# Kernel optimization log

Measured on AMD Instinct MI355X. Metric: run time of the kernel, lower is better.

## Reference

```python
import jax, jax.numpy as jnp
import numpy as np

IN_DIM = 512
OUT_DIM = 512
NUM_HARMONICS = 32
BATCH = 4096


def setup_inputs() -> dict:
    key = jax.random.key(0)
    k1, k2 = jax.random.split(key)
    x = jax.random.normal(k1, (BATCH, IN_DIM), dtype=jnp.float32)
    std = 1.0 / np.sqrt(IN_DIM * NUM_HARMONICS)
    fourier_coeffs = jax.random.normal(
        k2, (IN_DIM, NUM_HARMONICS, 2, OUT_DIM), dtype=jnp.float32) * std
    bias = jnp.zeros((OUT_DIM,), dtype=jnp.float32)
    return {"x": x, "fourier_coeffs": fourier_coeffs, "bias": bias}


def reference(x, fourier_coeffs, bias):
    # k = [1, ..., num_harmonics]
    k = jnp.arange(1, fourier_coeffs.shape[1] + 1, dtype=x.dtype)
    kx = x[:, :, None] * k                      # [b, i, g]
    trig = jnp.stack([jnp.cos(kx), jnp.sin(kx)], axis=-1)  # [b, i, g, 2]
    out = jnp.einsum('bigf,igfo->bo', trig, fourier_coeffs)
    return out + bias
```

## Files before the change

kernel.cpp:

```cpp
#include <hip/hip_runtime.h>
#include <hip/hip_bf16.h>
#include <stdint.h>
#include <stddef.h>

#define BATCH   4096
#define INDIM   512
#define OUTDIM  512
#define NH      32
#define KKDIM   64
#define INV2PI  0.15915494309189535f

#define BM       256
#define BN       256
#define THREADS  512
#define KSPLIT   8
#define DIMS_PER_WG (INDIM / KSPLIT)
#define CHUNK_ELEMS (BN * KKDIM)

#define B_BYTES   32768
#define A_BYTES   (BM * 128)
#define OFF_A0    (2 * B_BYTES)
#define OFF_X     (OFF_A0 + 2 * A_BYTES)
#define X_CHUNK_BYTES (8 * BM * 4)
#define SMEM_BYTES (OFF_X + 2 * X_CHUNK_BYTES)

typedef short  bhalf8  __attribute__((ext_vector_type(8)));
typedef float  vfloat4 __attribute__((ext_vector_type(4)));

__device__ __forceinline__ unsigned pack_bf16(float a, float b) {
    union { __hip_bfloat162 h2; unsigned u; } cv;
    cv.h2 = __float22bfloat162_rn(float2{a, b});
    return cv.u;
}

__device__ __forceinline__ void async_copy16(const void* gsrc, void* ldst) {
    __builtin_amdgcn_global_load_lds(
        (const __attribute__((address_space(1))) void*)(uintptr_t)gsrc,
        (__attribute__((address_space(3))) void*)(uint32_t)(uintptr_t)ldst,
        16, 0, 0);
}

__global__ __launch_bounds__(256) void fkan_prepass(const float* __restrict__ coeffs,
                                                    unsigned short* __restrict__ Bt) {
    __shared__ float lds[64][260];
    const int t  = threadIdx.x;
    const int cb = blockIdx.x & 1;
    const int i  = blockIdx.x >> 1;
    const float* __restrict__ src = coeffs + (size_t)i * (KKDIM * OUTDIM) + cb * BN;
    unsigned short* __restrict__ chunk = Bt + (size_t)(cb * INDIM + i) * CHUNK_ELEMS;
#pragma unroll
    for (int rd = 0; rd < 16; ++rd) {
        const int r  = rd * 4 + (t >> 6);
        const int c4 = (t & 63) * 4;
        const float4 v = *(const float4*)(src + (size_t)r * OUTDIM + c4);
        *(float4*)&lds[r][c4] = v;
    }
    __syncthreads();
#pragma unroll
    for (int s = 0; s < 8; ++s) {
        const int unit = t + s * 256;
        const int col  = unit >> 3;
        const int pc   = unit & 7;
        const int kb   = (pc ^ (col & 7)) * 8;
        uint4 o;
        o.x = pack_bf16(lds[kb + 0][col], lds[kb + 1][col]);
        o.y = pack_bf16(lds[kb + 2][col], lds[kb + 3][col]);
        o.z = pack_bf16(lds[kb + 4][col], lds[kb + 5][col]);
        o.w = pack_bf16(lds[kb + 6][col], lds[kb + 7][col]);
        ((uint4*)chunk)[unit] = o;
    }
}

__global__ __launch_bounds__(256) void fkan_bias_init(const float* __restrict__ bias,
                                                      float* __restrict__ out) {
    const int idx = blockIdx.x * 256 + threadIdx.x;
    ((float4*)out)[idx] = ((const float4*)bias)[idx & 127];
}

__device__ __forceinline__ void stage_B(const unsigned short* __restrict__ Bt, char* smem,
                                        int cb, int dim_global, int parity, int t) {
    const char* chunk = (const char*)(Bt + (size_t)(cb * INDIM + dim_global) * CHUNK_ELEMS);
    char* bdst = smem + parity * B_BYTES;
#pragma unroll
    for (int s = 0; s < 4; ++s) {
        const int unit = t + s * 512;
        async_copy16(chunk + unit * 16, bdst + unit * 16);
    }
}

__device__ __forceinline__ void stage_x(const float* __restrict__ x, char* smem,
                                        int rowbase, int dimbase, int cn, int t) {
    const int r  = t >> 1;
    const int d0 = (t & 1) * 4;
    const float4 xv = *(const float4*)(x + (size_t)(rowbase + r) * INDIM + dimbase + cn * 8 + d0);
    float* xr = (float*)(smem + OFF_X + (cn & 1) * X_CHUNK_BYTES);
    xr[(d0 + 0) * BM + r] = xv.x * INV2PI;
    xr[(d0 + 1) * BM + r] = xv.y * INV2PI;
    xr[(d0 + 2) * BM + r] = xv.z * INV2PI;
    xr[(d0 + 3) * BM + r] = xv.w * INV2PI;
}

__device__ __forceinline__ void do_trig(char* smem, int dim_local, int parity, int trow, int tq) {
    const float rv = ((const float*)(smem + OFF_X + ((dim_local >> 3) & 1) * X_CHUNK_BYTES))
                     [(dim_local & 7) * BM + trow];
    const float cd = __builtin_amdgcn_cosf(rv);
    const float sd = __builtin_amdgcn_sinf(rv);
    const float a0 = (float)(tq * 16 + 1) * rv;
    float c = __builtin_amdgcn_cosf(a0);
    float s = __builtin_amdgcn_sinf(a0);
    unsigned pk[16];
    pk[0] = pack_bf16(c, s);
#pragma unroll
    for (int j = 1; j < 16; ++j) {
        const float nc = c * cd - s * sd;
        const float ns = s * cd + c * sd;
        c = nc; s = ns;
        pk[j] = pack_bf16(c, s);
    }
    uint4* abase = (uint4*)(smem + OFF_A0 + parity * A_BYTES + trow * 128);
    const int sw = trow & 7;
    uint4 w0; w0.x = pk[0];  w0.y = pk[1];  w0.z = pk[2];  w0.w = pk[3];
    uint4 w1; w1.x = pk[4];  w1.y = pk[5];  w1.z = pk[6];  w1.w = pk[7];
    uint4 w2; w2.x = pk[8];  w2.y = pk[9];  w2.z = pk[10]; w2.w = pk[11];
    uint4 w3; w3.x = pk[12]; w3.y = pk[13]; w3.z = pk[14]; w3.w = pk[15];
    abase[(tq * 4 + 0) ^ sw] = w0;
    abase[(tq * 4 + 1) ^ sw] = w1;
    abase[(tq * 4 + 2) ^ sw] = w2;
    abase[(tq * 4 + 3) ^ sw] = w3;
}

__global__ __launch_bounds__(THREADS, 2) void fkan_main(const float* __restrict__ x,
                                                        const unsigned short* __restrict__ Bt,
                                                        float* __restrict__ out) {
    __shared__ char smem[SMEM_BYTES];
    const int t      = threadIdx.x;
    const int grp    = blockIdx.x & 15;
    const int member = blockIdx.x >> 4;
    const int cb      = grp & 1;
    const int kq      = grp >> 1;
    const int rowbase = member * BM;
    const int colbase = cb * BN;
    const int dimbase = kq * DIMS_PER_WG;

    const int lane = t & 63;
    const int w    = t >> 6;
    const int wr   = w >> 2;
    const int wc   = w & 3;
    const int fr   = lane & 15;
    const int fq   = lane >> 4;
    const int fx   = lane & 7;

    const int trow = t >> 1;
    const int tq   = t & 1;

    vfloat4 acc[8][4];
#pragma unroll
    for (int a = 0; a < 8; ++a)
#pragma unroll
        for (int b = 0; b < 4; ++b) acc[a][b] = (vfloat4)0.0f;

    stage_x(x, smem, rowbase, dimbase, 0, t);
    __syncthreads();
    stage_B(Bt, smem, cb, dimbase + 0, 0, t);
    do_trig(smem, 0, 0, trow, tq);
    __syncthreads();

#pragma unroll 2
    for (int it = 0; it < DIMS_PER_WG; ++it) {
        const int p    = it & 1;
        const int inxt = it + 1;
        if (inxt < DIMS_PER_WG) {
            stage_B(Bt, smem, cb, dimbase + inxt, inxt & 1, t);
            if ((it & 7) == 0) {
                const int cn = (it >> 3) + 1;
                if (cn < 8) stage_x(x, smem, rowbase, dimbase, cn, t);
            }
            do_trig(smem, inxt, inxt & 1, trow, tq);
        }
        {
            const char* Ab = smem + OFF_A0 + p * A_BYTES;
            const char* Bb = smem + p * B_BYTES;
#pragma unroll
            for (int ks = 0; ks < 2; ++ks) {
                bhalf8 bv[4];
#pragma unroll
                for (int ct = 0; ct < 4; ++ct)
                    bv[ct] = *(const bhalf8*)(Bb + (wc * 64 + ct * 16 + fr) * 128
                                                 + (((ks * 4 + fq) ^ fx) * 16));
#pragma unroll
                for (int rt = 0; rt < 8; ++rt) {
                    const bhalf8 av = *(const bhalf8*)(Ab + (wr * 128 + rt * 16 + fr) * 128
                                                          + (((ks * 4 + fq) ^ fx) * 16));
#pragma unroll
                    for (int ct = 0; ct < 4; ++ct)
                        acc[rt][ct] = __builtin_amdgcn_mfma_f32_16x16x32_bf16(
                            av, bv[ct], acc[rt][ct], 0, 0, 0);
                }
            }
        }
        __syncthreads();
    }

#pragma unroll
    for (int rt = 0; rt < 8; ++rt) {
#pragma unroll
        for (int ct = 0; ct < 4; ++ct) {
            const int col  = colbase + wc * 64 + ct * 16 + fr;
            const int row0 = rowbase + wr * 128 + rt * 16 + fq * 4;
#pragma unroll
            for (int r = 0; r < 4; ++r)
                atomicAdd(out + (size_t)(row0 + r) * OUTDIM + col, acc[rt][ct][r]);
        }
    }
}

__global__ __launch_bounds__(256) void fkan_naive(const float* __restrict__ x,
                                                  const float* __restrict__ coeffs,
                                                  const float* __restrict__ bias,
                                                  float* __restrict__ out) {
    const int b = blockIdx.x >> 1;
    const int o = ((blockIdx.x & 1) << 8) + threadIdx.x;
    float acc = bias[o];
    const float* xrow = x + (size_t)b * INDIM;
    for (int i = 0; i < INDIM; ++i) {
        const float rv = xrow[i] * INV2PI;
        const float cd = __builtin_amdgcn_cosf(rv);
        const float sd = __builtin_amdgcn_sinf(rv);
        float c = cd, s = sd;
        const float* cp = coeffs + (size_t)i * (KKDIM * OUTDIM) + o;
#pragma unroll 4
        for (int g = 0; g < NH; ++g) {
            acc += c * cp[g * 2 * OUTDIM] + s * cp[(g * 2 + 1) * OUTDIM];
            const float nc = c * cd - s * sd;
            const float ns = s * cd + c * sd;
            c = nc; s = ns;
        }
    }
    out[(size_t)b * OUTDIM + o] = acc;
}

extern "C" void kernel_launch(void* const* d_in, const int* in_sizes, int n_in,
                              void* d_out, int out_size, void* d_ws, size_t ws_size,
                              hipStream_t stream) {
    (void)in_sizes; (void)n_in; (void)out_size;
    const float* x      = (const float*)d_in[0];
    const float* coeffs = (const float*)d_in[1];
    const float* bias   = (const float*)d_in[2];
    float* out          = (float*)d_out;

    const size_t bt_bytes = (size_t)2 * INDIM * CHUNK_ELEMS * sizeof(unsigned short);
    if (ws_size >= bt_bytes) {
        unsigned short* Bt = (unsigned short*)d_ws;
        fkan_prepass<<<2 * INDIM, 256, 0, stream>>>(coeffs, Bt);
        fkan_bias_init<<<(BATCH * OUTDIM) / (4 * 256), 256, 0, stream>>>(bias, out);
        fkan_main<<<(BATCH / BM) * 2 * KSPLIT, THREADS, 0, stream>>>(x, Bt, out);
    } else {
        fkan_naive<<<BATCH * 2, 256, 0, stream>>>(x, coeffs, bias, out);
    }
}
```

Baseline: 277.1 us.

## Shrink tiles to 128x128 and load B fragments directly from global memory

Tiles shrink from 256x256 with 512 threads to 128x128 with 256 threads, and the grid grows to 1024 workgroups with a target of four per CU. B is no longer staged in LDS through async copies. Each wave loads its bf16 MFMA fragments straight from global memory, so the prepass drops its XOR swizzle. The change also adds s_setprio around the MFMA block, trading data reuse per tile for more occupancy and less LDS traffic and risking extra global and L2 load pressure.

```diff
diff --git a/kernel.cpp b/kernel.cpp
--- a/kernel.cpp
+++ b/kernel.cpp
@@ -10,19 +10,18 @@
 #define KKDIM   64
 #define INV2PI  0.15915494309189535f
 
-#define BM       256
-#define BN       256
-#define THREADS  512
+#define BM       128
+#define BN       128
+#define THREADS  256
 #define KSPLIT   8
 #define DIMS_PER_WG (INDIM / KSPLIT)
-#define CHUNK_ELEMS (BN * KKDIM)
-
-#define B_BYTES   32768
-#define A_BYTES   (BM * 128)
-#define OFF_A0    (2 * B_BYTES)
-#define OFF_X     (OFF_A0 + 2 * A_BYTES)
+#define CHUNK_COLS  256
+#define CHUNK_ELEMS (CHUNK_COLS * KKDIM)
+
+#define A_BYTES       (BM * 128)
+#define OFF_X         (2 * A_BYTES)
 #define X_CHUNK_BYTES (8 * BM * 4)
-#define SMEM_BYTES (OFF_X + 2 * X_CHUNK_BYTES)
+#define SMEM_BYTES    (OFF_X + 2 * X_CHUNK_BYTES)
 
 typedef short  bhalf8  __attribute__((ext_vector_type(8)));
 typedef float  vfloat4 __attribute__((ext_vector_type(4)));
@@ -31,13 +30,6 @@
     union { __hip_bfloat162 h2; unsigned u; } cv;
     cv.h2 = __float22bfloat162_rn(float2{a, b});
     return cv.u;
-}
-
-__device__ __forceinline__ void async_copy16(const void* gsrc, void* ldst) {
-    __builtin_amdgcn_global_load_lds(
-        (const __attribute__((address_space(1))) void*)(uintptr_t)gsrc,
-        (__attribute__((address_space(3))) void*)(uint32_t)(uintptr_t)ldst,
-        16, 0, 0);
 }
 
 __global__ __launch_bounds__(256) void fkan_prepass(const float* __restrict__ coeffs,
@@ -46,7 +38,7 @@
     const int t  = threadIdx.x;
     const int cb = blockIdx.x & 1;
     const int i  = blockIdx.x >> 1;
-    const float* __restrict__ src = coeffs + (size_t)i * (KKDIM * OUTDIM) + cb * BN;
+    const float* __restrict__ src = coeffs + (size_t)i * (KKDIM * OUTDIM) + cb * CHUNK_COLS;
     unsigned short* __restrict__ chunk = Bt + (size_t)(cb * INDIM + i) * CHUNK_ELEMS;
 #pragma unroll
     for (int rd = 0; rd < 16; ++rd) {
@@ -60,8 +52,7 @@
     for (int s = 0; s < 8; ++s) {
         const int unit = t + s * 256;
         const int col  = unit >> 3;
-        const int pc   = unit & 7;
-        const int kb   = (pc ^ (col & 7)) * 8;
+        const int kb   = (unit & 7) * 8;
         uint4 o;
         o.x = pack_bf16(lds[kb + 0][col], lds[kb + 1][col]);
         o.y = pack_bf16(lds[kb + 2][col], lds[kb + 3][col]);
@@ -75,17 +66,6 @@
                                                       float* __restrict__ out) {
     const int idx = blockIdx.x * 256 + threadIdx.x;
     ((float4*)out)[idx] = ((const float4*)bias)[idx & 127];
-}
-
-__device__ __forceinline__ void stage_B(const unsigned short* __restrict__ Bt, char* smem,
-                                        int cb, int dim_global, int parity, int t) {
-    const char* chunk = (const char*)(Bt + (size_t)(cb * INDIM + dim_global) * CHUNK_ELEMS);
-    char* bdst = smem + parity * B_BYTES;
-#pragma unroll
-    for (int s = 0; s < 4; ++s) {
-        const int unit = t + s * 512;
-        async_copy16(chunk + unit * 16, bdst + unit * 16);
-    }
 }
 
 __device__ __forceinline__ void stage_x(const float* __restrict__ x, char* smem,
@@ -117,7 +97,7 @@
         c = nc; s = ns;
         pk[j] = pack_bf16(c, s);
     }
-    uint4* abase = (uint4*)(smem + OFF_A0 + parity * A_BYTES + trow * 128);
+    uint4* abase = (uint4*)(smem + parity * A_BYTES + trow * 128);
     const int sw = trow & 7;
     uint4 w0; w0.x = pk[0];  w0.y = pk[1];  w0.z = pk[2];  w0.w = pk[3];
     uint4 w1; w1.x = pk[4];  w1.y = pk[5];  w1.z = pk[6];  w1.w = pk[7];
@@ -129,23 +109,24 @@
     abase[(tq * 4 + 3) ^ sw] = w3;
 }
 
-__global__ __launch_bounds__(THREADS, 2) void fkan_main(const float* __restrict__ x,
+__global__ __launch_bounds__(THREADS, 4) void fkan_main(const float* __restrict__ x,
                                                         const unsigned short* __restrict__ Bt,
                                                         float* __restrict__ out) {
     __shared__ char smem[SMEM_BYTES];
     const int t      = threadIdx.x;
-    const int grp    = blockIdx.x & 15;
-    const int member = blockIdx.x >> 4;
-    const int cb      = grp & 1;
-    const int kq      = grp >> 1;
+    const int grp    = blockIdx.x & 31;
+    const int member = blockIdx.x >> 5;
+    const int cb4     = grp & 3;
+    const int kq      = grp >> 2;
+    const int cb2     = cb4 >> 1;
     const int rowbase = member * BM;
-    const int colbase = cb * BN;
+    const int colbase = cb4 * BN;
     const int dimbase = kq * DIMS_PER_WG;
 
     const int lane = t & 63;
     const int w    = t >> 6;
-    const int wr   = w >> 2;
-    const int wc   = w & 3;
+    const int wr   = w >> 1;
+    const int wc   = w & 1;
     const int fr   = lane & 15;
     const int fq   = lane >> 4;
     const int fx   = lane & 7;
@@ -153,60 +134,81 @@
     const int trow = t >> 1;
     const int tq   = t & 1;
 
-    vfloat4 acc[8][4];
-#pragma unroll
-    for (int a = 0; a < 8; ++a)
+    const int boff = ((cb4 & 1) * 128 + wc * 64 + fr) * 128 + fq * 16;
+    const char* __restrict__ Bbase =
+        (const char*)(Bt + (size_t)(cb2 * INDIM + dimbase) * CHUNK_ELEMS) + boff;
+
+    vfloat4 acc[4][4];
+#pragma unroll
+    for (int a = 0; a < 4; ++a)
 #pragma unroll
         for (int b = 0; b < 4; ++b) acc[a][b] = (vfloat4)0.0f;
 
     stage_x(x, smem, rowbase, dimbase, 0, t);
     __syncthreads();
-    stage_B(Bt, smem, cb, dimbase + 0, 0, t);
     do_trig(smem, 0, 0, trow, tq);
     __syncthreads();
 
-#pragma unroll 2
     for (int it = 0; it < DIMS_PER_WG; ++it) {
         const int p    = it & 1;
         const int inxt = it + 1;
+        const char* Bc = Bbase + (size_t)it * (CHUNK_ELEMS * 2);
+
+        bhalf8 bv0[4];
+#pragma unroll
+        for (int ct = 0; ct < 4; ++ct)
+            bv0[ct] = *(const bhalf8*)(Bc + ct * (16 * 128));
+
         if (inxt < DIMS_PER_WG) {
-            stage_B(Bt, smem, cb, dimbase + inxt, inxt & 1, t);
             if ((it & 7) == 0) {
                 const int cn = (it >> 3) + 1;
                 if (cn < 8) stage_x(x, smem, rowbase, dimbase, cn, t);
             }
             do_trig(smem, inxt, inxt & 1, trow, tq);
         }
+
+        const char* Ab = smem + p * A_BYTES;
+        __builtin_amdgcn_s_setprio(1);
         {
-            const char* Ab = smem + OFF_A0 + p * A_BYTES;
-            const char* Bb = smem + p * B_BYTES;
-#pragma unroll
-            for (int ks = 0; ks < 2; ++ks) {
-                bhalf8 bv[4];
+            bhalf8 av[4];
+#pragma unroll
+            for (int rt = 0; rt < 4; ++rt)
+                av[rt] = *(const bhalf8*)(Ab + (wr * 64 + rt * 16 + fr) * 128
+                                             + ((fq ^ fx) * 16));
+#pragma unroll
+            for (int rt = 0; rt < 4; ++rt)
 #pragma unroll
                 for (int ct = 0; ct < 4; ++ct)
-                    bv[ct] = *(const bhalf8*)(Bb + (wc * 64 + ct * 16 + fr) * 128
-                                                 + (((ks * 4 + fq) ^ fx) * 16));
-#pragma unroll
-                for (int rt = 0; rt < 8; ++rt) {
-                    const bhalf8 av = *(const bhalf8*)(Ab + (wr * 128 + rt * 16 + fr) * 128
-                                                          + (((ks * 4 + fq) ^ fx) * 16));
-#pragma unroll
-                    for (int ct = 0; ct < 4; ++ct)
-                        acc[rt][ct] = __builtin_amdgcn_mfma_f32_16x16x32_bf16(
-                            av, bv[ct], acc[rt][ct], 0, 0, 0);
-                }
-            }
-        }
+                    acc[rt][ct] = __builtin_amdgcn_mfma_f32_16x16x32_bf16(
+                        av[rt], bv0[ct], acc[rt][ct], 0, 0, 0);
+        }
+        {
+            bhalf8 bv1[4];
+#pragma unroll
+            for (int ct = 0; ct < 4; ++ct)
+                bv1[ct] = *(const bhalf8*)(Bc + ct * (16 * 128) + 4 * 16);
+            bhalf8 av[4];
+#pragma unroll
+            for (int rt = 0; rt < 4; ++rt)
+                av[rt] = *(const bhalf8*)(Ab + (wr * 64 + rt * 16 + fr) * 128
+                                             + (((4 + fq) ^ fx) * 16));
+#pragma unroll
+            for (int rt = 0; rt < 4; ++rt)
+#pragma unroll
+                for (int ct = 0; ct < 4; ++ct)
+                    acc[rt][ct] = __builtin_amdgcn_mfma_f32_16x16x32_bf16(
+                        av[rt], bv1[ct], acc[rt][ct], 0, 0, 0);
+        }
+        __builtin_amdgcn_s_setprio(0);
         __syncthreads();
     }
 
 #pragma unroll
-    for (int rt = 0; rt < 8; ++rt) {
+    for (int rt = 0; rt < 4; ++rt) {
 #pragma unroll
         for (int ct = 0; ct < 4; ++ct) {
             const int col  = colbase + wc * 64 + ct * 16 + fr;
-            const int row0 = rowbase + wr * 128 + rt * 16 + fq * 4;
+            const int row0 = rowbase + wr * 64 + rt * 16 + fq * 4;
 #pragma unroll
             for (int r = 0; r < 4; ++r)
                 atomicAdd(out + (size_t)(row0 + r) * OUTDIM + col, acc[rt][ct][r]);
@@ -253,7 +255,7 @@
         unsigned short* Bt = (unsigned short*)d_ws;
         fkan_prepass<<<2 * INDIM, 256, 0, stream>>>(coeffs, Bt);
         fkan_bias_init<<<(BATCH * OUTDIM) / (4 * 256), 256, 0, stream>>>(bias, out);
-        fkan_main<<<(BATCH / BM) * 2 * KSPLIT, THREADS, 0, stream>>>(x, Bt, out);
+        fkan_main<<<(BATCH / BM) * (OUTDIM / BN) * KSPLIT, THREADS, 0, stream>>>(x, Bt, out);
     } else {
         fkan_naive<<<BATCH * 2, 256, 0, stream>>>(x, coeffs, bias, out);
     }
```

Result: slower. 363.9 us (+31.3%).
